# Kernel tuning notes

Measured on AMD Instinct MI355X. Metric: run time of the kernel, lower is better.

## Reference

```python
import jax, jax.numpy as jnp
import numpy as np

D_MODEL = 1024
NHEAD = 16
DH = D_MODEL // NHEAD  # 64
B, S = 4, 2048
SCALE = float(np.sqrt(D_MODEL))  # note: sqrt(d_model), not sqrt(dh)


def setup_inputs() -> dict:
    key = jax.random.key(0)
    ks = jax.random.split(key, 8)
    inputs = jax.random.normal(ks[0], (B, S, D_MODEL), dtype=jnp.float32)
    mask = jax.random.normal(ks[1], (B, S, S), dtype=jnp.float32) * 0.1
    # Linear weights stored as [in, out] so y = x @ W + b (equivalent to torch x @ W.T + b)
    std = 1.0 / np.sqrt(D_MODEL)
    Wq = jax.random.normal(ks[2], (D_MODEL, DH), dtype=jnp.float32) * std
    Wk = jax.random.normal(ks[3], (D_MODEL, DH), dtype=jnp.float32) * std
    Wv = jax.random.normal(ks[4], (D_MODEL, DH), dtype=jnp.float32) * std
    bq = jnp.zeros((DH,), dtype=jnp.float32)
    bk = jnp.zeros((DH,), dtype=jnp.float32)
    bv = jnp.zeros((DH,), dtype=jnp.float32)
    return {"inputs": inputs, "mask": mask, "Wq": Wq, "bq": bq,
            "Wk": Wk, "bk": bk, "Wv": Wv, "bv": bv}


def reference(inputs, mask, Wq, bq, Wk, bk, Wv, bv):
    # Projections: [B,S,d_model] -> [B,S,dh]
    Q = inputs @ Wq + bq
    K = inputs @ Wk + bk
    V = inputs @ Wv + bv
    # scores: [B, S_q, S_k]
    scores = jnp.einsum("bqd,bkd->bqk", Q, K) / SCALE
    # Faithful quirk: softmax over dim=1 (the QUERY axis), not the key axis
    probs = jax.nn.softmax(scores, axis=1)
    # Faithful quirk: mask added AFTER softmax
    A = jnp.einsum("bqk,bkd->bqd", probs + mask, V)
    return A
```

## Files before the change

kernel.cpp:

```cpp
#include <hip/hip_runtime.h>

#define NB 4
#define SS 2048
#define DMODEL 1024
#define DHEAD 64

typedef __bf16 bf16x8 __attribute__((ext_vector_type(8)));
typedef __bf16 bf16x4 __attribute__((ext_vector_type(4)));
typedef float f32x4 __attribute__((ext_vector_type(4)));

#define MFMA16(a, b, c) __builtin_amdgcn_mfma_f32_16x16x32_bf16((a), (b), (c), 0, 0, 0)


__global__ __launch_bounds__(256) void k0_wt3(
    const float* __restrict__ Wq, const float* __restrict__ Wk,
    const float* __restrict__ Wv, __bf16* __restrict__ Wt3)
{
    int idx = blockIdx.x * 256 + threadIdx.x;
    int kc = idx / 768;
    int rem = idx - kc * 768;
    int f = rem >> 6;
    int lane = rem & 63;
    int g = lane >> 4, l15 = lane & 15;
    int mode = f >> 2, nt = f & 3;
    const float* W = (mode == 0) ? Wq : (mode == 1 ? Wk : Wv);
    const float s = (mode == 0) ? 0.03125f : 1.0f;
    int n = nt * 16 + l15;
    int k = kc * 32 + g * 8;
    bf16x8 o;
    #pragma unroll
    for (int i = 0; i < 8; ++i)
        o[i] = (__bf16)(W[(size_t)(k + i) * DHEAD + n] * s);
    *(bf16x8*)(Wt3 + (size_t)idx * 8) = o;
}

#define XST 1032
__global__ __launch_bounds__(256) void k1_fused(
    const float* __restrict__ x, const __bf16* __restrict__ Wt3,
    const float* __restrict__ bq, const float* __restrict__ bk,
    const float* __restrict__ bv,
    __bf16* __restrict__ Qo, __bf16* __restrict__ Kb3, __bf16* __restrict__ Vt3)
{
    __shared__ char smem[36864];
    __bf16* stage = (__bf16*)smem;
    const int tid = threadIdx.x;
    const int wid = tid >> 6;
    const int lane = tid & 63;
    const int l15 = lane & 15;
    const int g = lane >> 4;
    const int row0 = blockIdx.x * 16;

    {
        const float* xsrc = x + (size_t)row0 * DMODEL;
        #pragma unroll
        for (int it = 0; it < 16; ++it) {
            int idx = it * 256 + tid;
            int row = idx >> 8;
            int col = (idx & 255) * 4;
            f32x4 v = *(const f32x4*)(xsrc + (size_t)row * DMODEL + col);
            bf16x4 b4;
            #pragma unroll
            for (int i = 0; i < 4; ++i) b4[i] = (__bf16)v[i];
            *(bf16x4*)(stage + row * XST + col) = b4;
        }
    }
    __syncthreads();

    f32x4 acc[12];
    #pragma unroll
    for (int f = 0; f < 12; ++f) acc[f] = (f32x4){0.f, 0.f, 0.f, 0.f};

    #pragma unroll
    for (int c = 0; c < 8; ++c) {
        bf16x8 af = *(const bf16x8*)(stage + l15 * XST + wid * 256 + c * 32 + g * 8);
        const int kc = wid * 8 + c;
        #pragma unroll
        for (int f = 0; f < 12; ++f) {
            bf16x8 bfr = *(const bf16x8*)(Wt3 + (((size_t)kc * 12 + f) << 9) + lane * 8);
            acc[f] = MFMA16(af, bfr, acc[f]);
        }
    }
    __syncthreads();
    f32x4* red = (f32x4*)smem;
    if (wid != 0) {
        #pragma unroll
        for (int f = 0; f < 12; ++f) red[((wid - 1) * 12 + f) * 64 + lane] = acc[f];
    }
    __syncthreads();
    if (wid == 0) {
        const int b  = row0 >> 11;
        const int s0 = row0 & 2047;
        const int soff = (s0 >> 3) & 2;
        #pragma unroll
        for (int f = 0; f < 12; ++f) {
            f32x4 a = acc[f] + red[(0 * 12 + f) * 64 + lane]
                    + red[(1 * 12 + f) * 64 + lane] + red[(2 * 12 + f) * 64 + lane];
            const int md = f >> 2, nt = f & 3;
            const int n = nt * 16 + l15;
            const float* bias = (md == 0) ? bq : (md == 1 ? bk : bv);
            const float bscale = (md == 0) ? 0.03125f : 1.0f;
            float bvl = bias[n] * bscale;
            #pragma unroll
            for (int r = 0; r < 4; ++r) {
                float o = a[r] + bvl;
                int sr = s0 + g * 4 + r;
                if (md == 0) {
                    Qo[((size_t)b * SS + sr) * DHEAD + n] = (__bf16)o;
                } else if (md == 1) {
                    size_t fid = (size_t)b * 256 + (s0 >> 4) * 2 + (nt >> 1);
                    int ln = ((nt & 1) * 2 + (l15 >> 3)) * 16 + g * 4 + r;
                    Kb3[(fid << 9) + ln * 8 + (l15 & 7)] = (__bf16)o;
                } else {
                    size_t fid = (size_t)b * 256 + (s0 >> 5) * 4 + nt;
                    int ln = (soff + ((g * 4 + r) >> 3)) * 16 + l15;
                    Vt3[(fid << 9) + ln * 8 + ((g * 4 + r) & 7)] = (__bf16)o;
                }
            }
        }
    }
}

#define QST 72
__global__ __launch_bounds__(256) void k2_cs(
    const __bf16* __restrict__ Qb, const __bf16* __restrict__ Kb3,
    float* __restrict__ partial)
{
    __shared__ __bf16 qt[128 * QST];
    const int tid = threadIdx.x;
    const int wid = tid >> 6;
    const int lane = tid & 63;
    const int l15 = lane & 15;
    const int g = lane >> 4;
    const int bx = blockIdx.x;
    const int b  = bx >> 8;
    const int rem = bx & 255;
    const int kg = rem >> 4;
    const int qs = rem & 15;
    const int k0 = kg * 128 + wid * 32;

    {
        const __bf16* qsrc = Qb + ((size_t)(b * SS + qs * 128)) * DHEAD;
        #pragma unroll
        for (int it = 0; it < 4; ++it) {
            int idx = it * 256 + tid;
            int row = idx >> 3;
            int col = (idx & 7) * 8;
            *(bf16x8*)(qt + row * QST + col) = *(const bf16x8*)(qsrc + (size_t)idx * 8);
        }
    }

    const __bf16* kfr = Kb3 + (((size_t)b * 256 + (k0 >> 4) * 2) << 9) + lane * 8;
    bf16x8 ka00 = *(const bf16x8*)(kfr);
    bf16x8 ka01 = *(const bf16x8*)(kfr + 512);
    bf16x8 ka10 = *(const bf16x8*)(kfr + 1024);
    bf16x8 ka11 = *(const bf16x8*)(kfr + 1536);
    __syncthreads();

    f32x4 cs0 = (f32x4){0.f, 0.f, 0.f, 0.f};
    f32x4 cs1 = (f32x4){0.f, 0.f, 0.f, 0.f};

    #pragma unroll 2
    for (int j = 0; j < 8; ++j) {
        const __bf16* qr = qt + (j * 16 + l15) * QST + g * 8;
        bf16x8 qb0 = *(const bf16x8*)(qr);
        bf16x8 qb1 = *(const bf16x8*)(qr + 32);
        f32x4 s0 = (f32x4){0.f, 0.f, 0.f, 0.f};
        s0 = MFMA16(ka00, qb0, s0);
        s0 = MFMA16(ka01, qb1, s0);
        f32x4 s1 = (f32x4){0.f, 0.f, 0.f, 0.f};
        s1 = MFMA16(ka10, qb0, s1);
        s1 = MFMA16(ka11, qb1, s1);
        #pragma unroll
        for (int r = 0; r < 4; ++r) {
            cs0[r] += __expf(s0[r]);
            cs1[r] += __expf(s1[r]);
        }
    }
    #pragma unroll
    for (int off = 1; off < 16; off <<= 1) {
        #pragma unroll
        for (int r = 0; r < 4; ++r) {
            cs0[r] += __shfl_xor(cs0[r], off);
            cs1[r] += __shfl_xor(cs1[r], off);
        }
    }
    if (l15 == 0) {
        float* pp = partial + (size_t)qs * (NB * SS) + b * SS + k0 + 4 * g;
        *(f32x4*)(pp)      = cs0;
        *(f32x4*)(pp + 16) = cs1;
    }
}

#define MST 2056
__global__ __launch_bounds__(256) void kab(
    const __bf16* __restrict__ Qb, const __bf16* __restrict__ Kb3,
    const __bf16* __restrict__ Vt3, const float* __restrict__ mask,
    const float* __restrict__ part, float* __restrict__ out)
{
    __shared__ char smem[16 * MST * 2 + 8192];
    __bf16* mt = (__bf16*)smem;
    float*  rl = (float*)(smem + 16 * MST * 2);
    const int tid = threadIdx.x;
    const int wid = tid >> 6;
    const int lane = tid & 63;
    const int l15 = lane & 15;
    const int g = lane >> 4;
    const int b  = blockIdx.x >> 7;
    const int q0 = (blockIdx.x & 127) * 16;

    {
        const int k = tid * 8;
        f32x4 sa = (f32x4){0.f, 0.f, 0.f, 0.f};
        f32x4 sb = (f32x4){0.f, 0.f, 0.f, 0.f};
        #pragma unroll
        for (int qs = 0; qs < 16; ++qs) {
            const float* pp = part + (size_t)qs * (NB * SS) + b * SS + k;
            sa += *(const f32x4*)(pp);
            sb += *(const f32x4*)(pp + 4);
        }
        f32x4 ra, rb;
        #pragma unroll
        for (int r = 0; r < 4; ++r) { ra[r] = 1.0f / sa[r]; rb[r] = 1.0f / sb[r]; }
        *(f32x4*)(rl + k) = ra;
        *(f32x4*)(rl + k + 4) = rb;
    }
    {
        const float* msrc = mask + ((size_t)(b * SS + q0)) * SS;
        #pragma unroll
        for (int it = 0; it < 32; ++it) {
            int idx = it * 256 + tid;
            int row = idx >> 9;
            int col = (idx & 511) * 4;
            f32x4 v = *(const f32x4*)(msrc + (size_t)row * SS + col);
            bf16x4 b4;
            #pragma unroll
            for (int i = 0; i < 4; ++i) b4[i] = (__bf16)v[i];
            *(bf16x4*)(mt + row * MST + col) = b4;
        }
    }

    const __bf16* qp = Qb + ((size_t)(b * SS + q0 + l15)) * DHEAD + g * 8;
    bf16x8 qb0 = *(const bf16x8*)(qp);
    bf16x8 qb1 = *(const bf16x8*)(qp + 32);
    __syncthreads();

    f32x4 acc[4];
    #pragma unroll
    for (int nt = 0; nt < 4; ++nt) acc[nt] = (f32x4){0.f, 0.f, 0.f, 0.f};

    #pragma unroll 2
    for (int st = 0; st < 16; ++st) {
        const int kbase = wid * 512 + st * 32;
        const __bf16* kfr = Kb3 + (((size_t)b * 256 + (kbase >> 4) * 2) << 9) + lane * 8;
        bf16x8 ka00 = *(const bf16x8*)(kfr);
        bf16x8 ka01 = *(const bf16x8*)(kfr + 512);
        bf16x8 ka10 = *(const bf16x8*)(kfr + 1024);
        bf16x8 ka11 = *(const bf16x8*)(kfr + 1536);
        const __bf16* vfr = Vt3 + (((size_t)b * 256 + (kbase >> 5) * 4) << 9) + lane * 8;
        bf16x8 vb0 = *(const bf16x8*)(vfr);
        bf16x8 vb1 = *(const bf16x8*)(vfr + 512);
        bf16x8 vb2 = *(const bf16x8*)(vfr + 1024);
        bf16x8 vb3 = *(const bf16x8*)(vfr + 1536);

        f32x4 s0 = (f32x4){0.f, 0.f, 0.f, 0.f};
        s0 = MFMA16(ka00, qb0, s0);
        s0 = MFMA16(ka01, qb1, s0);
        f32x4 s1 = (f32x4){0.f, 0.f, 0.f, 0.f};
        s1 = MFMA16(ka10, qb0, s1);
        s1 = MFMA16(ka11, qb1, s1);

        f32x4 rv0 = *(const f32x4*)(rl + kbase + 4 * g);
        f32x4 rv1 = *(const f32x4*)(rl + kbase + 16 + 4 * g);
        f32x4 e0, e1;
        #pragma unroll
        for (int r = 0; r < 4; ++r) {
            e0[r] = __expf(s0[r]) * rv0[r];
            e1[r] = __expf(s1[r]) * rv1[r];
        }
        bf16x8 mv = *(const bf16x8*)(mt + l15 * MST + kbase + g * 8);
        bf16x8 af;
        #pragma unroll
        for (int i = 0; i < 8; ++i) {
            int src = l15 + 16 * ((2 * g + (i >> 2)) & 3);
            float v0 = __shfl(e0[i & 3], src);
            float v1 = __shfl(e1[i & 3], src);
            af[i] = (__bf16)((g < 2 ? v0 : v1) + (float)mv[i]);
        }
        acc[0] = MFMA16(af, vb0, acc[0]);
        acc[1] = MFMA16(af, vb1, acc[1]);
        acc[2] = MFMA16(af, vb2, acc[2]);
        acc[3] = MFMA16(af, vb3, acc[3]);
    }
    __syncthreads();
    f32x4* red = (f32x4*)smem;
    #pragma unroll
    for (int nt = 0; nt < 4; ++nt) red[(wid * 4 + nt) * 64 + lane] = acc[nt];
    __syncthreads();
    if (wid == 0) {
        #pragma unroll
        for (int nt = 0; nt < 4; ++nt) {
            f32x4 a = red[(0 * 4 + nt) * 64 + lane] + red[(1 * 4 + nt) * 64 + lane]
                    + red[(2 * 4 + nt) * 64 + lane] + red[(3 * 4 + nt) * 64 + lane];
            #pragma unroll
            for (int r = 0; r < 4; ++r)
                out[((size_t)(b * SS + q0 + g * 4 + r)) * DHEAD + nt * 16 + l15] = a[r];
        }
    }
}

extern "C" void kernel_launch(void* const* d_in, const int* in_sizes, int n_in,
                              void* d_out, int out_size, void* d_ws, size_t ws_size,
                              hipStream_t stream)
{
    const float* x    = (const float*)d_in[0];
    const float* mask = (const float*)d_in[1];
    const float* Wq   = (const float*)d_in[2];
    const float* bq   = (const float*)d_in[3];
    const float* Wk   = (const float*)d_in[4];
    const float* bk   = (const float*)d_in[5];
    const float* Wv   = (const float*)d_in[6];
    const float* bv   = (const float*)d_in[7];
    float* out = (float*)d_out;

    char* ws = (char*)d_ws;
    __bf16* Qbf  = (__bf16*)(ws);
    __bf16* Kb3  = (__bf16*)(ws + (1u << 20));
    __bf16* Vt3  = (__bf16*)(ws + (2u << 20));
    float*  part = (float*)(ws + (3u << 20));
    __bf16* Wt3  = (__bf16*)(ws + (3u << 20) + (512u << 10));

    k0_wt3<<<96, 256, 0, stream>>>(Wq, Wk, Wv, Wt3);
    k1_fused<<<512, 256, 0, stream>>>(x, Wt3, bq, bk, bv, Qbf, Kb3, Vt3);
    k2_cs<<<1024, 256, 0, stream>>>(Qbf, Kb3, part);
    kab<<<512, 256, 0, stream>>>(Qbf, Kb3, Vt3, mask, part, out);
}
```

Baseline: 57.37 us.

## Stream mask directly into registers, widen kab to 512 threads, coalesce stores via LDS

The attention kernel no longer stages a 16x2048 mask tile in shared memory. Each lane loads mask values straight from global memory inside the loop and redistributes them with shuffles. Block size doubles to 8 waves, each covering half as many keys, which cuts shared memory use and should raise occupancy. Outputs of both the projection kernel and the attention kernel are staged in LDS so global writes become wide vector stores. The cost is more shuffles per element, an extra barrier, and a larger cross-wave reduction.

```diff
diff --git a/kernel.cpp b/kernel.cpp
--- a/kernel.cpp
+++ b/kernel.cpp
@@ -41,14 +41,20 @@
     const float* __restrict__ bv,
     __bf16* __restrict__ Qo, __bf16* __restrict__ Kb3, __bf16* __restrict__ Vt3)
 {
-    __shared__ char smem[36864];
+    __shared__ char smem[43008];
     __bf16* stage = (__bf16*)smem;
+    __bf16* outQ = (__bf16*)(smem + 36864);
+    __bf16* outK = outQ + 1024;
+    __bf16* outV = outK + 1024;
     const int tid = threadIdx.x;
     const int wid = tid >> 6;
     const int lane = tid & 63;
     const int l15 = lane & 15;
     const int g = lane >> 4;
     const int row0 = blockIdx.x * 16;
+    const int b  = row0 >> 11;
+    const int s0 = row0 & 2047;
+    const int soff = (s0 >> 3) & 2;
 
     {
         const float* xsrc = x + (size_t)row0 * DMODEL;
@@ -88,9 +94,6 @@
     }
     __syncthreads();
     if (wid == 0) {
-        const int b  = row0 >> 11;
-        const int s0 = row0 & 2047;
-        const int soff = (s0 >> 3) & 2;
         #pragma unroll
         for (int f = 0; f < 12; ++f) {
             f32x4 a = acc[f] + red[(0 * 12 + f) * 64 + lane]
@@ -103,20 +106,27 @@
             #pragma unroll
             for (int r = 0; r < 4; ++r) {
                 float o = a[r] + bvl;
-                int sr = s0 + g * 4 + r;
+                int g4r = g * 4 + r;
                 if (md == 0) {
-                    Qo[((size_t)b * SS + sr) * DHEAD + n] = (__bf16)o;
+                    outQ[g4r * 64 + n] = (__bf16)o;
                 } else if (md == 1) {
-                    size_t fid = (size_t)b * 256 + (s0 >> 4) * 2 + (nt >> 1);
-                    int ln = ((nt & 1) * 2 + (l15 >> 3)) * 16 + g * 4 + r;
-                    Kb3[(fid << 9) + ln * 8 + (l15 & 7)] = (__bf16)o;
+                    int ln = ((nt & 1) * 2 + (l15 >> 3)) * 16 + g4r;
+                    outK[(nt >> 1) * 512 + ln * 8 + (l15 & 7)] = (__bf16)o;
                 } else {
-                    size_t fid = (size_t)b * 256 + (s0 >> 5) * 4 + nt;
-                    int ln = (soff + ((g * 4 + r) >> 3)) * 16 + l15;
-                    Vt3[(fid << 9) + ln * 8 + ((g * 4 + r) & 7)] = (__bf16)o;
+                    outV[nt * 256 + ((g4r >> 3) * 16 + l15) * 8 + (g4r & 7)] = (__bf16)o;
                 }
             }
         }
+    }
+    __syncthreads();
+    if (tid < 128) {
+        *(bf16x8*)(Qo + ((size_t)b * SS + s0) * DHEAD + tid * 8) = *(bf16x8*)(outQ + tid * 8);
+        int nt = tid >> 5, e = (tid & 31) * 8;
+        *(bf16x8*)(Vt3 + (((size_t)(b * 256 + (s0 >> 5) * 4 + nt)) << 9) + soff * 128 + e)
+            = *(bf16x8*)(outV + nt * 256 + e);
+    } else {
+        int t2 = tid - 128;
+        *(bf16x8*)(Kb3 + (((size_t)b * 256 + (s0 >> 4) * 2) << 9) + t2 * 8) = *(bf16x8*)(outK + t2 * 8);
     }
 }
 
@@ -191,15 +201,14 @@
     }
 }
 
-#define MST 2056
-__global__ __launch_bounds__(256) void kab(
+__global__ __launch_bounds__(512) void kab(
     const __bf16* __restrict__ Qb, const __bf16* __restrict__ Kb3,
     const __bf16* __restrict__ Vt3, const float* __restrict__ mask,
     const float* __restrict__ part, float* __restrict__ out)
 {
-    __shared__ char smem[16 * MST * 2 + 8192];
-    __bf16* mt = (__bf16*)smem;
-    float*  rl = (float*)(smem + 16 * MST * 2);
+    __shared__ char smem[40960];
+    float* rl = (float*)smem;
+    f32x4* red = (f32x4*)(smem + 8192);
     const int tid = threadIdx.x;
     const int wid = tid >> 6;
     const int lane = tid & 63;
@@ -209,34 +218,15 @@
     const int q0 = (blockIdx.x & 127) * 16;
 
     {
-        const int k = tid * 8;
-        f32x4 sa = (f32x4){0.f, 0.f, 0.f, 0.f};
-        f32x4 sb = (f32x4){0.f, 0.f, 0.f, 0.f};
-        #pragma unroll
-        for (int qs = 0; qs < 16; ++qs) {
-            const float* pp = part + (size_t)qs * (NB * SS) + b * SS + k;
-            sa += *(const f32x4*)(pp);
-            sb += *(const f32x4*)(pp + 4);
-        }
-        f32x4 ra, rb;
-        #pragma unroll
-        for (int r = 0; r < 4; ++r) { ra[r] = 1.0f / sa[r]; rb[r] = 1.0f / sb[r]; }
-        *(f32x4*)(rl + k) = ra;
-        *(f32x4*)(rl + k + 4) = rb;
-    }
-    {
-        const float* msrc = mask + ((size_t)(b * SS + q0)) * SS;
-        #pragma unroll
-        for (int it = 0; it < 32; ++it) {
-            int idx = it * 256 + tid;
-            int row = idx >> 9;
-            int col = (idx & 511) * 4;
-            f32x4 v = *(const f32x4*)(msrc + (size_t)row * SS + col);
-            bf16x4 b4;
-            #pragma unroll
-            for (int i = 0; i < 4; ++i) b4[i] = (__bf16)v[i];
-            *(bf16x4*)(mt + row * MST + col) = b4;
-        }
+        const int k = tid * 4;
+        f32x4 s = (f32x4){0.f, 0.f, 0.f, 0.f};
+        #pragma unroll
+        for (int qs = 0; qs < 16; ++qs)
+            s += *(const f32x4*)(part + (size_t)qs * (NB * SS) + b * SS + k);
+        f32x4 rr;
+        #pragma unroll
+        for (int r = 0; r < 4; ++r) rr[r] = 1.0f / s[r];
+        *(f32x4*)(rl + k) = rr;
     }
 
     const __bf16* qp = Qb + ((size_t)(b * SS + q0 + l15)) * DHEAD + g * 8;
@@ -247,10 +237,12 @@
     f32x4 acc[4];
     #pragma unroll
     for (int nt = 0; nt < 4; ++nt) acc[nt] = (f32x4){0.f, 0.f, 0.f, 0.f};
+    const float* mrow = mask + ((size_t)(b * SS + q0 + (lane >> 2))) * SS + (lane & 3) * 8;
+    const int msrc = l15 * 4 + g;
 
     #pragma unroll 2
-    for (int st = 0; st < 16; ++st) {
-        const int kbase = wid * 512 + st * 32;
+    for (int st = 0; st < 8; ++st) {
+        const int kbase = wid * 256 + st * 32;
         const __bf16* kfr = Kb3 + (((size_t)b * 256 + (kbase >> 4) * 2) << 9) + lane * 8;
         bf16x8 ka00 = *(const bf16x8*)(kfr);
         bf16x8 ka01 = *(const bf16x8*)(kfr + 512);
@@ -261,6 +253,8 @@
         bf16x8 vb1 = *(const bf16x8*)(vfr + 512);
         bf16x8 vb2 = *(const bf16x8*)(vfr + 1024);
         bf16x8 vb3 = *(const bf16x8*)(vfr + 1536);
+        f32x4 mk0 = *(const f32x4*)(mrow + kbase);
+        f32x4 mk1 = *(const f32x4*)(mrow + kbase + 4);
 
         f32x4 s0 = (f32x4){0.f, 0.f, 0.f, 0.f};
         s0 = MFMA16(ka00, qb0, s0);
@@ -277,14 +271,14 @@
             e0[r] = __expf(s0[r]) * rv0[r];
             e1[r] = __expf(s1[r]) * rv1[r];
         }
-        bf16x8 mv = *(const bf16x8*)(mt + l15 * MST + kbase + g * 8);
         bf16x8 af;
         #pragma unroll
         for (int i = 0; i < 8; ++i) {
             int src = l15 + 16 * ((2 * g + (i >> 2)) & 3);
             float v0 = __shfl(e0[i & 3], src);
             float v1 = __shfl(e1[i & 3], src);
-            af[i] = (__bf16)((g < 2 ? v0 : v1) + (float)mv[i]);
+            float mval = __shfl((i < 4 ? mk0[i & 3] : mk1[i & 3]), msrc);
+            af[i] = (__bf16)((g < 2 ? v0 : v1) + mval);
         }
         acc[0] = MFMA16(af, vb0, acc[0]);
         acc[1] = MFMA16(af, vb1, acc[1]);
@@ -292,19 +286,24 @@
         acc[3] = MFMA16(af, vb3, acc[3]);
     }
     __syncthreads();
-    f32x4* red = (f32x4*)smem;
     #pragma unroll
     for (int nt = 0; nt < 4; ++nt) red[(wid * 4 + nt) * 64 + lane] = acc[nt];
     __syncthreads();
-    if (wid == 0) {
-        #pragma unroll
-        for (int nt = 0; nt < 4; ++nt) {
-            f32x4 a = red[(0 * 4 + nt) * 64 + lane] + red[(1 * 4 + nt) * 64 + lane]
-                    + red[(2 * 4 + nt) * 64 + lane] + red[(3 * 4 + nt) * 64 + lane];
-            #pragma unroll
-            for (int r = 0; r < 4; ++r)
-                out[((size_t)(b * SS + q0 + g * 4 + r)) * DHEAD + nt * 16 + l15] = a[r];
-        }
+    float* outO = (float*)smem;
+    if (wid < 4) {
+        const int nt = wid;
+        f32x4 a = red[nt * 64 + lane];
+        #pragma unroll
+        for (int w = 1; w < 8; ++w) a += red[(w * 4 + nt) * 64 + lane];
+        #pragma unroll
+        for (int r = 0; r < 4; ++r)
+            outO[(g * 4 + r) * 64 + nt * 16 + l15] = a[r];
+    }
+    __syncthreads();
+    if (tid < 256) {
+        int row = tid >> 4, col = (tid & 15) * 4;
+        *(f32x4*)(out + ((size_t)(b * SS + q0 + row)) * DHEAD + col)
+            = *(const f32x4*)(outO + row * 64 + col);
     }
 }
 
@@ -332,5 +331,5 @@
     k0_wt3<<<96, 256, 0, stream>>>(Wq, Wk, Wv, Wt3);
     k1_fused<<<512, 256, 0, stream>>>(x, Wt3, bq, bk, bv, Qbf, Kb3, Vt3);
     k2_cs<<<1024, 256, 0, stream>>>(Qbf, Kb3, part);
-    kab<<<512, 256, 0, stream>>>(Qbf, Kb3, Vt3, mask, part, out);
-}
+    kab<<<512, 512, 0, stream>>>(Qbf, Kb3, Vt3, mask, part, out);
+}
```

Result: faster. 54.92 us, median of 2 (-4.3%).
